# Kernel optimization log

Measured on AMD Instinct MI355X. Metric: run time of the kernel, lower is better.

Reference implementation:

```python
import jax, jax.numpy as jnp
import numpy as np

B, C_IN, C_OUT, H, W = 64, 1024, 1024, 16, 16
HEADS, C_RED = 8, 512  # reduced_ch = 1024 // 2
N = H * W
EPS = 1e-5  # BatchNorm eps (eval mode, running stats)
NEG_SLOPE = 0.2  # PyG GATConv default leaky_relu slope


def build_grid_edge_index(P, Pw):
    # 4-neighbor grid + one self-loop per node, directed [2, E]
    edges = []
    for i in range(P):
        for j in range(Pw):
            u = i * Pw + j
            if i - 1 >= 0: edges.append([u, u - Pw])
            if i + 1 < P:  edges.append([u, u + Pw])
            if j - 1 >= 0: edges.append([u, u - 1])
            if j + 1 < Pw: edges.append([u, u + 1])
            edges.append([u, u])
    return jnp.asarray(np.array(edges, dtype=np.int32).T)


def setup_inputs() -> dict:
    key = jax.random.key(0)
    ks = jax.random.split(key, 10)
    x = jax.random.normal(ks[0], (B, C_IN, H, W), jnp.float32)
    w_reduce = jax.random.normal(ks[1], (C_RED, C_IN), jnp.float32) * 0.02
    g_red = jnp.ones((C_RED,), jnp.float32); b_red = jnp.zeros((C_RED,), jnp.float32)
    m_red = jax.random.normal(ks[2], (C_RED,), jnp.float32) * 0.1
    v_red = jax.random.uniform(ks[3], (C_RED,), jnp.float32) + 0.5
    w_gat = jax.random.normal(ks[4], (C_RED, HEADS * C_RED), jnp.float32) * 0.02
    att_src = jax.random.normal(ks[5], (HEADS, C_RED), jnp.float32) * 0.1
    att_dst = jax.random.normal(ks[6], (HEADS, C_RED), jnp.float32) * 0.1
    gat_bias = jnp.zeros((C_RED,), jnp.float32)
    w_restore = jax.random.normal(ks[7], (C_OUT, C_RED), jnp.float32) * 0.02
    g_res = jnp.ones((C_OUT,), jnp.float32); b_res = jnp.zeros((C_OUT,), jnp.float32)
    m_res = jax.random.normal(ks[8], (C_OUT,), jnp.float32) * 0.1
    v_res = jax.random.uniform(ks[9], (C_OUT,), jnp.float32) + 0.5
    edge_index = build_grid_edge_index(H, W)
    return dict(x=x, w_reduce=w_reduce, g_red=g_red, b_red=b_red, m_red=m_red, v_red=v_red,
                w_gat=w_gat, att_src=att_src, att_dst=att_dst, gat_bias=gat_bias,
                w_restore=w_restore, g_res=g_res, b_res=b_res, m_res=m_res, v_res=v_res,
                edge_index=edge_index)


def _bn(x, g, b, m, v):  # channel-last, eval mode
    return (x - m) * (g * jax.lax.rsqrt(v + EPS)) + b


def reference(x, w_reduce, g_red, b_red, m_red, v_red, w_gat, att_src, att_dst,
              gat_bias, w_restore, g_res, b_res, m_res, v_res, edge_index):
    xh = jnp.transpose(x, (0, 2, 3, 1))                 # [B,H,W,C_in] NHWC
    res = xh                                            # identity residual (C_in == C_out)
    xr = jax.nn.relu(_bn(xh @ w_reduce.T, g_red, b_red, m_red, v_red))  # [B,H,W,C_red]
    nodes = xr.reshape(B, N, C_RED)                     # per-sample grid graph nodes

    # --- GATConv (heads=HEADS, concat=False), batched over B ---
    xp = (nodes @ w_gat).reshape(B, N, HEADS, C_RED)    # projected per-head features
    a_src = jnp.einsum('bnhc,hc->bnh', xp, att_src)
    a_dst = jnp.einsum('bnhc,hc->bnh', xp, att_dst)
    src, dst = edge_index[0], edge_index[1]
    logits = jax.nn.leaky_relu(a_src[:, src] + a_dst[:, dst], NEG_SLOPE)  # [B,E,HEADS]
    seg_max = jax.vmap(lambda a: jax.ops.segment_max(a, dst, num_segments=N))(logits)
    e = jnp.exp(logits - seg_max[:, dst])
    seg_sum = jax.vmap(lambda a: jax.ops.segment_sum(a, dst, num_segments=N))(e)
    alpha = e / seg_sum[:, dst]                          # softmax over incoming edges
    msg = alpha[..., None] * xp[:, src]                  # [B,E,HEADS,C_red]
    agg = jax.vmap(lambda m_: jax.ops.segment_sum(m_, dst, num_segments=N))(msg)
    gat_out = agg.mean(axis=2) + gat_bias                # concat=False -> head mean, [B,N,C_red]

    out = gat_out.reshape(B, H, W, C_RED) @ w_restore.T  # 1x1 restore conv
    out = _bn(out, g_res, b_res, m_res, v_res)
    out = jax.nn.relu(out + res)
    return jnp.transpose(out, (0, 3, 1, 2))              # [B,C_out,H,W]
```

## Files before the change

### kernel.cpp

```cpp
#include <hip/hip_runtime.h>


typedef unsigned short u16;
typedef __attribute__((ext_vector_type(4))) unsigned short u16x4;
typedef __attribute__((ext_vector_type(8))) unsigned short u16x8;
typedef __attribute__((ext_vector_type(8))) __bf16 bf16x8;
typedef __attribute__((ext_vector_type(2))) __bf16 bf16x2;
typedef __attribute__((ext_vector_type(4))) float f32x4;

#if defined(__has_builtin)
#if __has_builtin(__builtin_amdgcn_fdot2_f32_bf16)
#define HAVE_DOT2 1
#endif
#endif

#define B_    64
#define CIN   1024
#define CRED  512
#define COUT  1024
#define NPIX  256
#define HEADS 8
#define KGAT  4096
#define MTOT  16384
#define EPSB  1e-5f

__device__ __forceinline__ float b2f(u16 u) {
  union { unsigned u; float f; } c; c.u = ((unsigned)u) << 16; return c.f;
}
__device__ __forceinline__ u16 f2b(float f) {
  union { float f; unsigned u; } c; c.f = f;
  unsigned r = (c.u + 0x7FFFu + ((c.u >> 16) & 1u)) >> 16;
  return (u16)r;
}

__device__ __forceinline__ void gload_lds16(const void* g, void* lds) {
  __builtin_amdgcn_global_load_lds(
      (const __attribute__((address_space(1))) void*)g,
      (__attribute__((address_space(3))) void*)lds, 16, 0, 0);
}

union U8u {
  u16x8 v;
  bf16x2 p[4];
};

__global__ __launch_bounds__(256) void alphapre_kernel(
    const float* __restrict__ a_all, u16* __restrict__ alf_g)
{
  const int nh = blockIdx.x * 256 + threadIdx.x;
  const int ng = nh >> 3, h = nh & 7;
  const int n = ng & 255;
  const size_t nbase = (size_t)(ng >> 8) * NPIX;
  const int gi = n >> 4, gj = n & 15;
  int vv[5];
  vv[0] = n;
  vv[1] = (gi > 0)  ? n - 16 : -1;
  vv[2] = (gi < 15) ? n + 16 : -1;
  vv[3] = (gj > 0)  ? n - 1  : -1;
  vv[4] = (gj < 15) ? n + 1  : -1;
  const float* a_src = a_all;
  const float* a_dst = a_all + (size_t)MTOT * HEADS;
  const float ad = a_dst[(nbase + n) * HEADS + h];
  float l[5]; float mx = -1e30f;
#pragma unroll
  for (int e = 0; e < 5; ++e) {
    if (vv[e] >= 0) {
      const float xx = a_src[(nbase + vv[e]) * HEADS + h] + ad;
      l[e] = xx > 0.f ? xx : 0.2f * xx;
      mx = fmaxf(mx, l[e]);
    } else l[e] = -1e30f;
  }
  float s = 0.f, ee[5];
#pragma unroll
  for (int e = 0; e < 5; ++e) {
    ee[e] = (vv[e] >= 0) ? __expf(l[e] - mx) : 0.f;
    s += ee[e];
  }
  const float inv = 0.125f / s;
#pragma unroll
  for (int e = 0; e < 5; ++e)
    alf_g[(size_t)ng * 40 + e * 8 + h] = f2b(ee[e] * inv);
}

__global__ __launch_bounds__(512, 1) void gemm8p_kernel(
    const u16* __restrict__ A, const u16* __restrict__ Btp,
    const u16* __restrict__ alf_g, const float* __restrict__ gat_bias,
    u16* __restrict__ gat)
{
  extern __shared__ u16 lds[];
  u16* Ys  = lds;
  u16* alf = lds + 67584;

  const int tid = threadIdx.x;
  const int wave = tid >> 6, lane = tid & 63;
  const int wm = wave >> 2, wn = wave & 3;
  const int l15 = lane & 15, l4 = lane >> 4;

  int lin = blockIdx.y * 16 + blockIdx.x;
  lin = (lin & 7) * 128 + (lin >> 3);
  const int m0 = (lin >> 4) * 256;
  const int n0 = (lin & 15) * 256;
  const int img = lin >> 4;
  const int jbg = (lin & 15) * 32;
  const size_t nbase = (size_t)img * NPIX;

  int offS[2], ldsS[2];
#pragma unroll
  for (int i = 0; i < 2; ++i) {
    const int f = i * 512 + tid;
    const int r = f >> 2;
    const int kb = (f & 3) ^ ((r >> 1) & 3);
    offS[i] = r * 512 + kb * 8;
    ldsS[i] = (i * 512 + wave * 64) * 8;
  }
  const u16* gA = A + (size_t)m0 * 512;
  const u16* gB = Btp + (size_t)n0 * 512;

  auto stageA = [&](int kt) {
    const int bo = (kt & 3) * 16384;
    gload_lds16(gA + kt * 32 + offS[0], &lds[bo + ldsS[0]]);
    gload_lds16(gA + kt * 32 + offS[1], &lds[bo + ldsS[1]]);
  };
  auto stageB = [&](int kt) {
    const int bo = (kt & 3) * 16384 + 8192;
    gload_lds16(gB + kt * 32 + offS[0], &lds[bo + ldsS[0]]);
    gload_lds16(gB + kt * 32 + offS[1], &lds[bo + ldsS[1]]);
  };

  stageA(0); stageB(0); stageA(1); stageB(1);
  {
    const u16* ag = alf_g + nbase * 40;
    for (int i = tid; i < 1280; i += 512)
      *(u16x8*)&alf[i * 8] = *(const u16x8*)&ag[i * 8];
  }

  f32x4 acc[8][4];
#pragma unroll
  for (int i = 0; i < 8; ++i)
#pragma unroll
    for (int j = 0; j < 4; ++j) acc[i][j] = f32x4{0.f, 0.f, 0.f, 0.f};

  const int kq = (l4 ^ ((l15 >> 1) & 3)) * 8;
  const int aBase = (wm * 128 + l15) * 32 + kq;
  const int bBase = 8192 + (wn * 64 + l15) * 32 + kq;

  __syncthreads();

  for (int kt = 0; kt < 16; ++kt) {
    if (kt > 0) {
      if (kt == 15) { asm volatile("s_waitcnt vmcnt(0)" ::: "memory"); }
      else         { asm volatile("s_waitcnt vmcnt(4)" ::: "memory"); }
      __builtin_amdgcn_s_barrier();
    }
    const int bo = (kt & 3) * 16384;
    bf16x8 bfr[4], af0[4], af1[4];
#pragma unroll
    for (int f = 0; f < 4; ++f)
      bfr[f] = *(const bf16x8*)&lds[bo + bBase + f * 512];
#pragma unroll
    for (int f = 0; f < 4; ++f)
      af0[f] = *(const bf16x8*)&lds[bo + aBase + f * 512];
#pragma unroll
    for (int f = 0; f < 4; ++f)
      af1[f] = *(const bf16x8*)&lds[bo + aBase + (f + 4) * 512];
    if (kt < 14) { stageA(kt + 2); stageB(kt + 2); }
    __builtin_amdgcn_s_setprio(1);
#pragma unroll
    for (int fm = 0; fm < 4; ++fm)
#pragma unroll
      for (int fn = 0; fn < 4; ++fn)
        acc[fm][fn] = __builtin_amdgcn_mfma_f32_16x16x32_bf16(
            bfr[fn], af0[fm], acc[fm][fn], 0, 0, 0);
#pragma unroll
    for (int fm = 0; fm < 4; ++fm)
#pragma unroll
      for (int fn = 0; fn < 4; ++fn)
        acc[fm + 4][fn] = __builtin_amdgcn_mfma_f32_16x16x32_bf16(
            bfr[fn], af1[fm], acc[fm + 4][fn], 0, 0, 0);
    __builtin_amdgcn_s_setprio(0);
  }
  asm volatile("s_waitcnt vmcnt(0)" ::: "memory");
  __builtin_amdgcn_s_barrier();

#pragma unroll
  for (int fm = 0; fm < 8; ++fm) {
    const int nloc = wm * 128 + fm * 16 + l15;
#pragma unroll
    for (int fn = 0; fn < 4; ++fn) {
      const int cloc = wn * 64 + fn * 16 + l4 * 4;
      u16x4 ov;
#pragma unroll
      for (int r = 0; r < 4; ++r) ov[r] = f2b(acc[fm][fn][r]);
      *(u16x4*)&Ys[nloc * 264 + cloc] = ov;
    }
  }
  __syncthreads();

  const int b = tid & 7;
  const int nb8 = (tid >> 3) & 63;
  float fb[4];
#pragma unroll
  for (int k = 0; k < 4; ++k) fb[k] = gat_bias[jbg + b + 8 * k];
#pragma unroll
  for (int nn = 0; nn < 4; ++nn) {
    const int n = nb8 + nn * 64;
    const int gi = n >> 4, gj = n & 15;
    int vv[5];
    vv[0] = n;
    vv[1] = (gi > 0)  ? n - 16 : n;
    vv[2] = (gi < 15) ? n + 16 : n;
    vv[3] = (gj > 0)  ? n - 1  : n;
    vv[4] = (gj < 15) ? n + 1  : n;
    float o[4] = { fb[0], fb[1], fb[2], fb[3] };
#pragma unroll
    for (int e = 0; e < 5; ++e) {
      U8u au;
      au.v = *(const u16x8*)&alf[n * 40 + e * 8];
      const u16* yrow = &Ys[vv[e] * 264];
#if defined(HAVE_DOT2)
#pragma unroll
      for (int k = 0; k < 4; ++k) {
        U8u yu;
        yu.v = *(const u16x8*)&yrow[(b + 8 * k) * 8];
        float s = o[k];
        s = __builtin_amdgcn_fdot2_f32_bf16(yu.p[0], au.p[0], s, false);
        s = __builtin_amdgcn_fdot2_f32_bf16(yu.p[1], au.p[1], s, false);
        s = __builtin_amdgcn_fdot2_f32_bf16(yu.p[2], au.p[2], s, false);
        s = __builtin_amdgcn_fdot2_f32_bf16(yu.p[3], au.p[3], s, false);
        o[k] = s;
      }
#else
      float a8[8];
#pragma unroll
      for (int h = 0; h < 8; ++h) a8[h] = b2f(au.v[h]);
#pragma unroll
      for (int k = 0; k < 4; ++k) {
        const u16x8 yv = *(const u16x8*)&yrow[(b + 8 * k) * 8];
#pragma unroll
        for (int h = 0; h < 8; ++h) o[k] += a8[h] * b2f(yv[h]);
      }
#endif
    }
    const size_t gr = (nbase + n) * (size_t)CRED + jbg;
#pragma unroll
    for (int k = 0; k < 4; ++k) gat[gr + b + 8 * k] = f2b(o[k]);
  }
}

__global__ __launch_bounds__(512, 1) void gemm_res2_kernel(
    const u16* __restrict__ A, const u16* __restrict__ Bt,
    float* __restrict__ out32,
    const float* __restrict__ pg, const float* __restrict__ pb,
    const float* __restrict__ pm, const float* __restrict__ pv,
    const float* __restrict__ auxf)
{
  extern __shared__ u16 lds[];
  const int tid = threadIdx.x;
  const int wave = tid >> 6, lane = tid & 63;
  const int wm = wave >> 2, wn = wave & 3;
  const int l15 = lane & 15, l4 = lane >> 4;

  int lin = blockIdx.y * 4 + blockIdx.x;
  lin = (lin & 7) * 32 + (lin >> 3);
  const int m0 = (lin >> 2) * 256;
  const int n0 = (lin & 3) * 256;

  int offS[2], ldsS[2];
#pragma unroll
  for (int i = 0; i < 2; ++i) {
    const int f = i * 512 + tid;
    const int r = f >> 2;
    const int kb = (f & 3) ^ ((r >> 1) & 3);
    offS[i] = r * 512 + kb * 8;
    ldsS[i] = (i * 512 + wave * 64) * 8;
  }
  const u16* gA = A + (size_t)m0 * 512;
  const u16* gB = Bt + (size_t)n0 * 512;

  auto stageA = [&](int kt) {
    const int bo = (kt & 3) * 16384;
    gload_lds16(gA + kt * 32 + offS[0], &lds[bo + ldsS[0]]);
    gload_lds16(gA + kt * 32 + offS[1], &lds[bo + ldsS[1]]);
  };
  auto stageB = [&](int kt) {
    const int bo = (kt & 3) * 16384 + 8192;
    gload_lds16(gB + kt * 32 + offS[0], &lds[bo + ldsS[0]]);
    gload_lds16(gB + kt * 32 + offS[1], &lds[bo + ldsS[1]]);
  };

  f32x4 acc[8][4];
#pragma unroll
  for (int i = 0; i < 8; ++i)
#pragma unroll
    for (int j = 0; j < 4; ++j) acc[i][j] = f32x4{0.f, 0.f, 0.f, 0.f};

  const int kq = (l4 ^ ((l15 >> 1) & 3)) * 8;
  const int aBase = (wm * 128 + l15) * 32 + kq;
  const int bBase = 8192 + (wn * 64 + l15) * 32 + kq;

  stageA(0); stageB(0); stageA(1); stageB(1);

  for (int kt = 0; kt < 16; ++kt) {
    if (kt == 15) { asm volatile("s_waitcnt vmcnt(0)" ::: "memory"); }
    else         { asm volatile("s_waitcnt vmcnt(4)" ::: "memory"); }
    __builtin_amdgcn_s_barrier();
    const int bo = (kt & 3) * 16384;
    bf16x8 bfr[4], af0[4], af1[4];
#pragma unroll
    for (int f = 0; f < 4; ++f)
      bfr[f] = *(const bf16x8*)&lds[bo + bBase + f * 512];
#pragma unroll
    for (int f = 0; f < 4; ++f)
      af0[f] = *(const bf16x8*)&lds[bo + aBase + f * 512];
#pragma unroll
    for (int f = 0; f < 4; ++f)
      af1[f] = *(const bf16x8*)&lds[bo + aBase + (f + 4) * 512];
    if (kt < 14) { stageA(kt + 2); stageB(kt + 2); }
    __builtin_amdgcn_s_setprio(1);
#pragma unroll
    for (int fm = 0; fm < 4; ++fm)
#pragma unroll
      for (int fn = 0; fn < 4; ++fn)
        acc[fm][fn] = __builtin_amdgcn_mfma_f32_16x16x32_bf16(
            af0[fm], bfr[fn], acc[fm][fn], 0, 0, 0);
#pragma unroll
    for (int fm = 0; fm < 4; ++fm)
#pragma unroll
      for (int fn = 0; fn < 4; ++fn)
        acc[fm + 4][fn] = __builtin_amdgcn_mfma_f32_16x16x32_bf16(
            af1[fm], bfr[fn], acc[fm + 4][fn], 0, 0, 0);
    __builtin_amdgcn_s_setprio(0);
  }

  const int rowb = m0 + wm * 128 + l4 * 4;
#pragma unroll
  for (int fn = 0; fn < 4; ++fn) {
    const int col = n0 + wn * 64 + fn * 16 + l15;
    const float sc = pg[col] * rsqrtf(pv[col] + EPSB);
    const float off = pb[col] - pm[col] * sc;
#pragma unroll
    for (int fm = 0; fm < 8; ++fm) {
      const int row = rowb + fm * 16;
      const int bimg = row >> 8, p0 = row & 255;
      const size_t oa = (size_t)bimg * (COUT * NPIX) + (size_t)col * NPIX + p0;
      const float4 rv = *(const float4*)&auxf[oa];
      float4 ov;
      ov.x = fmaxf(acc[fm][fn][0] * sc + off + rv.x, 0.f);
      ov.y = fmaxf(acc[fm][fn][1] * sc + off + rv.y, 0.f);
      ov.z = fmaxf(acc[fm][fn][2] * sc + off + rv.z, 0.f);
      ov.w = fmaxf(acc[fm][fn][3] * sc + off + rv.w, 0.f);
      *(float4*)&out32[oa] = ov;
    }
  }
}

__global__ __launch_bounds__(256) void wgatp_kernel(
    const float* __restrict__ w_gat, u16* __restrict__ out)
{
  __shared__ float tile[64][65];
  const int cb = blockIdx.x;
  const int kb = blockIdx.y;
  const int t = threadIdx.x;
  const int jl = t & 7, h = (t >> 3) & 7, k4 = t >> 6;
#pragma unroll
  for (int i = 0; i < 16; ++i) {
    const int kl = k4 * 16 + i;
    tile[kl][jl * 8 + h] =
        w_gat[(size_t)(kb * 64 + kl) * KGAT + h * 512 + cb * 8 + jl];
  }
  __syncthreads();
#pragma unroll
  for (int i = 0; i < 4; ++i) {
    const int idx = i * 256 + t;
    const int cl = idx >> 4;
    const int kq = (idx & 15) * 4;
    u16x4 ov;
#pragma unroll
    for (int q = 0; q < 4; ++q) ov[q] = f2b(tile[kq + q][cl]);
    *(u16x4*)&out[(size_t)(cb * 64 + cl) * CRED + kb * 64 + kq] = ov;
  }
}

__global__ __launch_bounds__(256, 2) void gemm_redf_kernel(
    const float* __restrict__ x, const u16* __restrict__ Bt,
    u16* __restrict__ out16,
    const float* __restrict__ pg, const float* __restrict__ pb,
    const float* __restrict__ pm, const float* __restrict__ pv)
{
  __shared__ u16 As[64 * 32];
  __shared__ u16 Bs[128 * 32];
  const int tid = threadIdx.x;
  const int wave = tid >> 6, lane = tid & 63;
  const int gx = gridDim.x;
  const int nwg = gx * gridDim.y;
  int lin = blockIdx.y * gx + blockIdx.x;
  lin = (lin & 7) * (nwg >> 3) + (lin >> 3);
  const int m0 = (lin / gx) * 64, n0 = (lin % gx) * 128;
  const int bimg = m0 >> 8, p0 = m0 & 255;

  const float* xsrc = x + (size_t)bimg * CIN * NPIX + p0 + lane;

  int offB[2], dstB[2];
#pragma unroll
  for (int i = 0; i < 2; ++i) {
    const int f = i * 256 + tid;
    const int r = f >> 2;
    const int kb = (f & 3) ^ ((r >> 1) & 3);
    offB[i] = r * CIN + kb * 8;
    dstB[i] = (i * 256 + wave * 64) * 8;
  }
  const u16* gB = Bt + (size_t)n0 * CIN;

  const int aWr = (lane * 4 + (wave ^ ((lane >> 1) & 3))) * 8;

  f32x4 acc[2][4];
#pragma unroll
  for (int i = 0; i < 2; ++i)
#pragma unroll
    for (int j = 0; j < 4; ++j) acc[i][j] = f32x4{0.f, 0.f, 0.f, 0.f};

  const int wr = wave >> 1, wc = wave & 1;
  const int l15 = lane & 15, l4 = lane >> 4;
  const int kq = (l4 ^ ((l15 >> 1) & 3)) * 8;

  float av[8];
#pragma unroll
  for (int j = 0; j < 8; ++j) av[j] = xsrc[(wave * 8 + j) * NPIX];

  for (int kt = 0; kt < CIN; kt += 32) {
    u16x8 pvv;
#pragma unroll
    for (int j = 0; j < 8; ++j) pvv[j] = f2b(av[j]);
    *(u16x8*)&As[aWr] = pvv;
    gload_lds16(gB + kt + offB[0], &Bs[dstB[0]]);
    gload_lds16(gB + kt + offB[1], &Bs[dstB[1]]);
    __syncthreads();
    if (kt + 32 < CIN) {
#pragma unroll
      for (int j = 0; j < 8; ++j)
        av[j] = xsrc[(kt + 32 + wave * 8 + j) * NPIX];
    }
    bf16x8 af[2], bfr[4];
#pragma unroll
    for (int f = 0; f < 2; ++f)
      af[f] = *(const bf16x8*)&As[(wr * 32 + f * 16 + l15) * 32 + kq];
#pragma unroll
    for (int f = 0; f < 4; ++f)
      bfr[f] = *(const bf16x8*)&Bs[(wc * 64 + f * 16 + l15) * 32 + kq];
#pragma unroll
    for (int fm = 0; fm < 2; ++fm)
#pragma unroll
      for (int fn = 0; fn < 4; ++fn)
        acc[fm][fn] = __builtin_amdgcn_mfma_f32_16x16x32_bf16(
            af[fm], bfr[fn], acc[fm][fn], 0, 0, 0);
    __syncthreads();
  }

  const int rowb = m0 + wr * 32 + (lane >> 4) * 4;
#pragma unroll
  for (int fn = 0; fn < 4; ++fn) {
    const int col = n0 + wc * 64 + fn * 16 + l15;
    const float sc = pg[col] * rsqrtf(pv[col] + EPSB);
    const float off = pb[col] - pm[col] * sc;
#pragma unroll
    for (int fm = 0; fm < 2; ++fm) {
      const int row = rowb + fm * 16;
#pragma unroll
      for (int r = 0; r < 4; ++r) {
        const float y = fmaxf(acc[fm][fn][r] * sc + off, 0.f);
        out16[(size_t)(row + r) * CRED + col] = f2b(y);
      }
    }
  }
}

__global__ __launch_bounds__(256) void cvt2_kernel(
    const float* __restrict__ s0, u16* __restrict__ d0,
    const float* __restrict__ s1, u16* __restrict__ d1, int half)
{
  const int bi = blockIdx.x;
  const float* src = (bi < half) ? s0 : s1;
  u16* dst = (bi < half) ? d0 : d1;
  const int i = ((bi < half ? bi : bi - half) * 256 + threadIdx.x) * 8;
  const float4 a = *(const float4*)&src[i];
  const float4 b = *(const float4*)&src[i + 4];
  u16x8 o;
  o[0] = f2b(a.x); o[1] = f2b(a.y); o[2] = f2b(a.z); o[3] = f2b(a.w);
  o[4] = f2b(b.x); o[5] = f2b(b.y); o[6] = f2b(b.z); o[7] = f2b(b.w);
  *(u16x8*)&dst[i] = o;
}

__global__ __launch_bounds__(128) void attproj_kernel(
    const float* __restrict__ w_gat, const float* __restrict__ att_src,
    const float* __restrict__ att_dst, float* __restrict__ P)
{
  __shared__ float av[CRED];
  const int bi = blockIdx.x;
  const int sh = bi & 15, q = bi >> 4;
  const int s = sh >> 3, h = sh & 7;
  const float* att = (s == 0) ? att_src : att_dst;
  for (int t = threadIdx.x; t < CRED; t += 128) av[t] = att[h * CRED + t];
  __syncthreads();
  const int c = q * 128 + threadIdx.x;
  const float* wrow = w_gat + (size_t)c * KGAT + h * CRED;
  float acc = 0.f;
  for (int j = 0; j < CRED; j += 4) {
    const float4 w = *(const float4*)&wrow[j];
    acc += w.x * av[j] + w.y * av[j + 1] + w.z * av[j + 2] + w.w * av[j + 3];
  }
  P[(size_t)sh * CRED + c] = acc;
}

__global__ __launch_bounds__(256) void att_kernel(
    const u16* __restrict__ xr, const float* __restrict__ P,
    float* __restrict__ a_all)
{
  const int wave = threadIdx.x >> 6, lane = threadIdx.x & 63;
  const int m = blockIdx.x * 4 + wave;
  const int sh = lane & 15, q = lane >> 4;
  const u16* xp = xr + (size_t)m * CRED + q * 128;
  const float* Pp = P + (size_t)sh * CRED + q * 128;
  float s = 0.f;
#pragma unroll
  for (int c = 0; c < 128; c += 8) {
    u16x8 xv = *(const u16x8*)&xp[c];
#pragma unroll
    for (int t = 0; t < 8; ++t) s += b2f(xv[t]) * Pp[c + t];
  }
  s += __shfl_xor(s, 16);
  s += __shfl_xor(s, 32);
  if (q == 0)
    a_all[(size_t)(sh >> 3) * MTOT * HEADS + (size_t)m * HEADS + (sh & 7)] = s;
}

extern "C" void kernel_launch(void* const* d_in, const int* in_sizes, int n_in,
                              void* d_out, int out_size, void* d_ws, size_t ws_size,
                              hipStream_t stream)
{
  const float* x         = (const float*)d_in[0];
  const float* w_reduce  = (const float*)d_in[1];
  const float* g_red     = (const float*)d_in[2];
  const float* b_red     = (const float*)d_in[3];
  const float* m_red     = (const float*)d_in[4];
  const float* v_red     = (const float*)d_in[5];
  const float* w_gat     = (const float*)d_in[6];
  const float* att_src   = (const float*)d_in[7];
  const float* att_dst   = (const float*)d_in[8];
  const float* gat_bias  = (const float*)d_in[9];
  const float* w_restore = (const float*)d_in[10];
  const float* g_res     = (const float*)d_in[11];
  const float* b_res     = (const float*)d_in[12];
  const float* m_res     = (const float*)d_in[13];
  const float* v_res     = (const float*)d_in[14];

  constexpr size_t SZ_XR   = (size_t)MTOT * CRED * 2;
  constexpr size_t SZ_GAT  = SZ_XR;
  constexpr size_t SZ_WGT  = (size_t)KGAT * CRED * 2;
  constexpr size_t SZ_WRD  = (size_t)CRED * CIN * 2;
  constexpr size_t SZ_WRS  = (size_t)COUT * CRED * 2;
  constexpr size_t SZ_P    = (size_t)16 * CRED * 4;
  constexpr size_t SZ_AALL = (size_t)2 * MTOT * HEADS * 4;
  char* ws = (char*)d_ws;
  u16*   xr     = (u16*)ws;
  u16*   gat    = (u16*)(ws + SZ_XR);
  u16*   WgT2p  = (u16*)(ws + SZ_XR + SZ_GAT);
  u16*   wred_b = (u16*)(ws + SZ_XR + SZ_GAT + SZ_WGT);
  u16*   wres_b = (u16*)(ws + SZ_XR + SZ_GAT + SZ_WGT + SZ_WRD);
  float* P      = (float*)(ws + SZ_XR + SZ_GAT + SZ_WGT + SZ_WRD + SZ_WRS);
  float* a_all  = (float*)(ws + SZ_XR + SZ_GAT + SZ_WGT + SZ_WRD + SZ_WRS + SZ_P);
  u16*   alf_g  = (u16*)(ws + SZ_XR + SZ_GAT + SZ_WGT + SZ_WRD + SZ_WRS + SZ_P + SZ_AALL);
  float* outp   = (float*)d_out;

  hipFuncSetAttribute((const void*)gemm8p_kernel,
                      hipFuncAttributeMaxDynamicSharedMemorySize, 155648);
  hipFuncSetAttribute((const void*)gemm_res2_kernel,
                      hipFuncAttributeMaxDynamicSharedMemorySize, 131072);

  wgatp_kernel<<<dim3(64, 8), 256, 0, stream>>>(w_gat, WgT2p);
  cvt2_kernel<<<512, 256, 0, stream>>>(
      w_reduce, wred_b, w_restore, wres_b, 256);
  gemm_redf_kernel<<<dim3(4, 256), 256, 0, stream>>>(
      x, wred_b, xr, g_red, b_red, m_red, v_red);
  attproj_kernel<<<64, 128, 0, stream>>>(w_gat, att_src, att_dst, P);
  att_kernel<<<MTOT / 4, 256, 0, stream>>>(xr, P, a_all);
  alphapre_kernel<<<512, 256, 0, stream>>>(a_all, alf_g);
  gemm8p_kernel<<<dim3(16, 64), 512, 155648, stream>>>(
      xr, WgT2p, alf_g, gat_bias, gat);
  gemm_res2_kernel<<<dim3(4, 64), 512, 131072, stream>>>(
      gat, wres_b, outp, g_res, b_res, m_res, v_res, x);
  (void)in_sizes; (void)n_in; (void)out_size; (void)ws_size;
}
```

Before: 243.1 us.

## Shrink fused GAT GEMM tile to 256x128 with double buffering for higher occupancy

Replaces the 256x256 fused GAT projection+aggregation kernel with a 256x128 tile version launched as 2048 blocks, using 2-stage LDS buffering instead of 4-stage and a much smaller LDS footprint so more blocks can be resident per CU. The alpha weights are now read directly from global into registers instead of staged in LDS, and the epilogue assigns each thread one node and eight output channels with a single vector store. The aim is better latency hiding through occupancy. The cost is a full vmcnt(0) wait every k-step with less prefetch depth, and more blocks re-reading A tiles across the N dimension.

```diff
diff --git a/kernel.cpp b/kernel.cpp
--- a/kernel.cpp
+++ b/kernel.cpp
@@ -82,169 +82,152 @@
     alf_g[(size_t)ng * 40 + e * 8 + h] = f2b(ee[e] * inv);
 }
 
-__global__ __launch_bounds__(512, 1) void gemm8p_kernel(
+__global__ __launch_bounds__(512, 4) void gemmf2_kernel(
     const u16* __restrict__ A, const u16* __restrict__ Btp,
     const u16* __restrict__ alf_g, const float* __restrict__ gat_bias,
     u16* __restrict__ gat)
 {
   extern __shared__ u16 lds[];
-  u16* Ys  = lds;
-  u16* alf = lds + 67584;
+  u16* Ys = lds;
 
   const int tid = threadIdx.x;
   const int wave = tid >> 6, lane = tid & 63;
-  const int wm = wave >> 2, wn = wave & 3;
+  const int wm = wave >> 1, wn = wave & 1;
   const int l15 = lane & 15, l4 = lane >> 4;
 
-  int lin = blockIdx.y * 16 + blockIdx.x;
-  lin = (lin & 7) * 128 + (lin >> 3);
-  const int m0 = (lin >> 4) * 256;
-  const int n0 = (lin & 15) * 256;
-  const int img = lin >> 4;
-  const int jbg = (lin & 15) * 32;
+  const int raw = blockIdx.x;
+  const int lin = (raw & 7) * 256 + (raw >> 3);
+  const int img = lin >> 5;
+  const int ntile = lin & 31;
+  const int n0 = ntile * 128;
+  const int jbg = ntile * 16;
   const size_t nbase = (size_t)img * NPIX;
 
-  int offS[2], ldsS[2];
+  int offA[2], dstA[2];
 #pragma unroll
   for (int i = 0; i < 2; ++i) {
     const int f = i * 512 + tid;
     const int r = f >> 2;
     const int kb = (f & 3) ^ ((r >> 1) & 3);
-    offS[i] = r * 512 + kb * 8;
-    ldsS[i] = (i * 512 + wave * 64) * 8;
-  }
-  const u16* gA = A + (size_t)m0 * 512;
+    offA[i] = r * 512 + kb * 8;
+    dstA[i] = (i * 512 + wave * 64) * 8;
+  }
+  const int rB = tid >> 2;
+  const int kbB = (tid & 3) ^ ((rB >> 1) & 3);
+  const int offB = rB * 512 + kbB * 8;
+  const int dstB = wave * 64 * 8;
+
+  const u16* gA = A + (size_t)img * 256 * 512;
   const u16* gB = Btp + (size_t)n0 * 512;
 
-  auto stageA = [&](int kt) {
-    const int bo = (kt & 3) * 16384;
-    gload_lds16(gA + kt * 32 + offS[0], &lds[bo + ldsS[0]]);
-    gload_lds16(gA + kt * 32 + offS[1], &lds[bo + ldsS[1]]);
+  auto stage = [&](int t) {
+    const int d = (t & 1) * 12288;
+    gload_lds16(gA + t * 32 + offA[0], &lds[d + dstA[0]]);
+    gload_lds16(gA + t * 32 + offA[1], &lds[d + dstA[1]]);
+    gload_lds16(gB + t * 32 + offB, &lds[d + 8192 + dstB]);
   };
-  auto stageB = [&](int kt) {
-    const int bo = (kt & 3) * 16384 + 8192;
-    gload_lds16(gB + kt * 32 + offS[0], &lds[bo + ldsS[0]]);
-    gload_lds16(gB + kt * 32 + offS[1], &lds[bo + ldsS[1]]);
-  };
-
-  stageA(0); stageB(0); stageA(1); stageB(1);
-  {
-    const u16* ag = alf_g + nbase * 40;
-    for (int i = tid; i < 1280; i += 512)
-      *(u16x8*)&alf[i * 8] = *(const u16x8*)&ag[i * 8];
-  }
-
-  f32x4 acc[8][4];
-#pragma unroll
-  for (int i = 0; i < 8; ++i)
+
+  f32x4 acc[4][4];
+#pragma unroll
+  for (int i = 0; i < 4; ++i)
 #pragma unroll
     for (int j = 0; j < 4; ++j) acc[i][j] = f32x4{0.f, 0.f, 0.f, 0.f};
 
   const int kq = (l4 ^ ((l15 >> 1) & 3)) * 8;
-  const int aBase = (wm * 128 + l15) * 32 + kq;
+  const int aBase = (wm * 64 + l15) * 32 + kq;
   const int bBase = 8192 + (wn * 64 + l15) * 32 + kq;
 
-  __syncthreads();
-
-  for (int kt = 0; kt < 16; ++kt) {
-    if (kt > 0) {
-      if (kt == 15) { asm volatile("s_waitcnt vmcnt(0)" ::: "memory"); }
-      else         { asm volatile("s_waitcnt vmcnt(4)" ::: "memory"); }
-      __builtin_amdgcn_s_barrier();
-    }
-    const int bo = (kt & 3) * 16384;
-    bf16x8 bfr[4], af0[4], af1[4];
-#pragma unroll
-    for (int f = 0; f < 4; ++f)
-      bfr[f] = *(const bf16x8*)&lds[bo + bBase + f * 512];
-#pragma unroll
-    for (int f = 0; f < 4; ++f)
-      af0[f] = *(const bf16x8*)&lds[bo + aBase + f * 512];
-#pragma unroll
-    for (int f = 0; f < 4; ++f)
-      af1[f] = *(const bf16x8*)&lds[bo + aBase + (f + 4) * 512];
-    if (kt < 14) { stageA(kt + 2); stageB(kt + 2); }
+  stage(0);
+
+  for (int t = 0; t < 16; ++t) {
+    asm volatile("s_waitcnt vmcnt(0)" ::: "memory");
+    __builtin_amdgcn_s_barrier();
+    const int d = (t & 1) * 12288;
+    bf16x8 af[4], bfr[4];
+#pragma unroll
+    for (int f = 0; f < 4; ++f) {
+      af[f]  = *(const bf16x8*)&lds[d + aBase + f * 512];
+      bfr[f] = *(const bf16x8*)&lds[d + bBase + f * 512];
+    }
+    if (t < 15) stage(t + 1);
     __builtin_amdgcn_s_setprio(1);
 #pragma unroll
     for (int fm = 0; fm < 4; ++fm)
 #pragma unroll
       for (int fn = 0; fn < 4; ++fn)
         acc[fm][fn] = __builtin_amdgcn_mfma_f32_16x16x32_bf16(
-            bfr[fn], af0[fm], acc[fm][fn], 0, 0, 0);
-#pragma unroll
-    for (int fm = 0; fm < 4; ++fm)
-#pragma unroll
-      for (int fn = 0; fn < 4; ++fn)
-        acc[fm + 4][fn] = __builtin_amdgcn_mfma_f32_16x16x32_bf16(
-            bfr[fn], af1[fm], acc[fm + 4][fn], 0, 0, 0);
+            bfr[fn], af[fm], acc[fm][fn], 0, 0, 0);
     __builtin_amdgcn_s_setprio(0);
   }
-  asm volatile("s_waitcnt vmcnt(0)" ::: "memory");
-  __builtin_amdgcn_s_barrier();
-
-#pragma unroll
-  for (int fm = 0; fm < 8; ++fm) {
-    const int nloc = wm * 128 + fm * 16 + l15;
+  __syncthreads();
+
+#pragma unroll
+  for (int fm = 0; fm < 4; ++fm) {
+    const int nloc = wm * 64 + fm * 16 + l15;
 #pragma unroll
     for (int fn = 0; fn < 4; ++fn) {
       const int cloc = wn * 64 + fn * 16 + l4 * 4;
       u16x4 ov;
 #pragma unroll
       for (int r = 0; r < 4; ++r) ov[r] = f2b(acc[fm][fn][r]);
-      *(u16x4*)&Ys[nloc * 264 + cloc] = ov;
+      *(u16x4*)&Ys[nloc * 136 + cloc] = ov;
     }
   }
   __syncthreads();
 
-  const int b = tid & 7;
-  const int nb8 = (tid >> 3) & 63;
-  float fb[4];
-#pragma unroll
-  for (int k = 0; k < 4; ++k) fb[k] = gat_bias[jbg + b + 8 * k];
-#pragma unroll
-  for (int nn = 0; nn < 4; ++nn) {
-    const int n = nb8 + nn * 64;
-    const int gi = n >> 4, gj = n & 15;
-    int vv[5];
-    vv[0] = n;
-    vv[1] = (gi > 0)  ? n - 16 : n;
-    vv[2] = (gi < 15) ? n + 16 : n;
-    vv[3] = (gj > 0)  ? n - 1  : n;
-    vv[4] = (gj < 15) ? n + 1  : n;
-    float o[4] = { fb[0], fb[1], fb[2], fb[3] };
-#pragma unroll
-    for (int e = 0; e < 5; ++e) {
-      U8u au;
-      au.v = *(const u16x8*)&alf[n * 40 + e * 8];
-      const u16* yrow = &Ys[vv[e] * 264];
+  const int n = tid >> 1, half = tid & 1;
+  const int gi = n >> 4, gj = n & 15;
+  int vv[5];
+  vv[0] = n;
+  vv[1] = (gi > 0)  ? n - 16 : n;
+  vv[2] = (gi < 15) ? n + 16 : n;
+  vv[3] = (gj > 0)  ? n - 1  : n;
+  vv[4] = (gj < 15) ? n + 1  : n;
+  U8u au[5];
+  {
+    const u16* ag = alf_g + (nbase + n) * 40;
+#pragma unroll
+    for (int e = 0; e < 5; ++e) au[e].v = *(const u16x8*)&ag[e * 8];
+  }
+  float o[8];
+  {
+    const int jb = jbg + half * 8;
+    const float4 b0 = *(const float4*)&gat_bias[jb];
+    const float4 b1 = *(const float4*)&gat_bias[jb + 4];
+    o[0] = b0.x; o[1] = b0.y; o[2] = b0.z; o[3] = b0.w;
+    o[4] = b1.x; o[5] = b1.y; o[6] = b1.z; o[7] = b1.w;
+  }
+#pragma unroll
+  for (int e = 0; e < 5; ++e) {
+    const u16* yrow = &Ys[vv[e] * 136 + half * 64];
 #if defined(HAVE_DOT2)
 #pragma unroll
-      for (int k = 0; k < 4; ++k) {
-        U8u yu;
-        yu.v = *(const u16x8*)&yrow[(b + 8 * k) * 8];
-        float s = o[k];
-        s = __builtin_amdgcn_fdot2_f32_bf16(yu.p[0], au.p[0], s, false);
-        s = __builtin_amdgcn_fdot2_f32_bf16(yu.p[1], au.p[1], s, false);
-        s = __builtin_amdgcn_fdot2_f32_bf16(yu.p[2], au.p[2], s, false);
-        s = __builtin_amdgcn_fdot2_f32_bf16(yu.p[3], au.p[3], s, false);
-        o[k] = s;
-      }
+    for (int k = 0; k < 8; ++k) {
+      U8u yu;
+      yu.v = *(const u16x8*)&yrow[k * 8];
+      float s = o[k];
+      s = __builtin_amdgcn_fdot2_f32_bf16(yu.p[0], au[e].p[0], s, false);
+      s = __builtin_amdgcn_fdot2_f32_bf16(yu.p[1], au[e].p[1], s, false);
+      s = __builtin_amdgcn_fdot2_f32_bf16(yu.p[2], au[e].p[2], s, false);
+      s = __builtin_amdgcn_fdot2_f32_bf16(yu.p[3], au[e].p[3], s, false);
+      o[k] = s;
+    }
 #else
-      float a8[8];
-#pragma unroll
-      for (int h = 0; h < 8; ++h) a8[h] = b2f(au.v[h]);
-#pragma unroll
-      for (int k = 0; k < 4; ++k) {
-        const u16x8 yv = *(const u16x8*)&yrow[(b + 8 * k) * 8];
-#pragma unroll
-        for (int h = 0; h < 8; ++h) o[k] += a8[h] * b2f(yv[h]);
-      }
+    float a8[8];
+#pragma unroll
+    for (int h = 0; h < 8; ++h) a8[h] = b2f(au[e].v[h]);
+#pragma unroll
+    for (int k = 0; k < 8; ++k) {
+      const u16x8 yv = *(const u16x8*)&yrow[k * 8];
+#pragma unroll
+      for (int h = 0; h < 8; ++h) o[k] += a8[h] * b2f(yv[h]);
+    }
 #endif
-    }
-    const size_t gr = (nbase + n) * (size_t)CRED + jbg;
-#pragma unroll
-    for (int k = 0; k < 4; ++k) gat[gr + b + 8 * k] = f2b(o[k]);
-  }
+  }
+  u16x8 ov;
+#pragma unroll
+  for (int k = 0; k < 8; ++k) ov[k] = f2b(o[k]);
+  *(u16x8*)&gat[(nbase + n) * (size_t)CRED + jbg + half * 8] = ov;
 }
 
 __global__ __launch_bounds__(512, 1) void gemm_res2_kernel(
@@ -571,8 +554,8 @@
   u16*   alf_g  = (u16*)(ws + SZ_XR + SZ_GAT + SZ_WGT + SZ_WRD + SZ_WRS + SZ_P + SZ_AALL);
   float* outp   = (float*)d_out;
 
-  hipFuncSetAttribute((const void*)gemm8p_kernel,
-                      hipFuncAttributeMaxDynamicSharedMemorySize, 155648);
+  hipFuncSetAttribute((const void*)gemmf2_kernel,
+                      hipFuncAttributeMaxDynamicSharedMemorySize, 69632);
   hipFuncSetAttribute((const void*)gemm_res2_kernel,
                       hipFuncAttributeMaxDynamicSharedMemorySize, 131072);
 
@@ -584,7 +567,7 @@
   attproj_kernel<<<64, 128, 0, stream>>>(w_gat, att_src, att_dst, P);
   att_kernel<<<MTOT / 4, 256, 0, stream>>>(xr, P, a_all);
   alphapre_kernel<<<512, 256, 0, stream>>>(a_all, alf_g);
-  gemm8p_kernel<<<dim3(16, 64), 512, 155648, stream>>>(
+  gemmf2_kernel<<<2048, 512, 69632, stream>>>(
       xr, WgT2p, alf_g, gat_bias, gat);
   gemm_res2_kernel<<<dim3(4, 64), 512, 131072, stream>>>(
       gat, wres_b, outp, g_res, b_res, m_res, v_res, x);
```

Result: faster. 236.4 us (-2.8%).
